# Optimization experiments

Hardware: AMD Instinct MI355X
Metric: run time of the kernel (lower is better)

Reference implementation:

```python
import jax, jax.numpy as jnp
import numpy as np
from jax import lax

NFILT = 80
NBINS = 257  # nfft//2 + 1


def build_filterbank(binpoints):
    """Vectorized version of the nested-loop triangular filterbank build.
    Matches torch semantics: bin ranges use int() (trunc==floor for positive
    values) of the sorted learnable binpoints; last filter row (j=nfilt-1)
    is never written and stays zero.
    """
    b = jnp.sort(binpoints)
    ib = jnp.floor(b).astype(jnp.int32)
    i = jnp.arange(NBINS)
    fi = i.astype(b.dtype)
    bj, bj1, bj2 = b[:NFILT, None], b[1:NFILT + 1, None], b[2:NFILT + 2, None]
    ibj, ibj1, ibj2 = ib[:NFILT, None], ib[1:NFILT + 1, None], ib[2:NFILT + 2, None]
    rise_m = (i >= ibj) & (i < ibj1)
    fall_m = (i >= ibj1) & (i < ibj2)
    d1 = (bj1 - bj) ** 2
    d2 = (bj2 - bj1) ** 2
    rise = (fi - bj) / jnp.where(d1 > 0, d1, 1.0)
    fall = (bj2 - fi) / jnp.where(d2 > 0, d2, 1.0)
    fb = jnp.where(rise_m, rise, jnp.where(fall_m, fall, 0.0))
    row_ok = (jnp.arange(NFILT) < NFILT - 1)[:, None]  # loop runs j in [0, nfilt-1)
    return fb * row_ok  # [80, 257]


def dconv1d(h, w, b, dilation, pad):
    # h: [B, C, T], w: [O, I, K]
    y = lax.conv_general_dilated(h, w, window_strides=(1,), padding=[(pad, pad)],
                                 rhs_dilation=(dilation,),
                                 dimension_numbers=('NCH', 'OIH', 'NCH'))
    return y + b[None, :, None]


def setup_inputs() -> dict:
    key = jax.random.key(0)
    ks = jax.random.split(key, 20)
    B, T = 64, 3000
    f32 = jnp.float32
    x = jax.random.normal(ks[0], (B, T, NBINS), dtype=f32)
    # distinct sorted binpoints in [1, 257) as in torch init (randint then sort)
    binpoints = jnp.sort(jax.random.choice(ks[1], jnp.arange(1, NBINS), (NFILT + 2,), replace=False).astype(f32))
    def lin(k, o, i):
        return jax.random.normal(k, (o, i), dtype=f32) * (1.0 / np.sqrt(i))
    def conv_w(k, o, i, ksz):
        return jax.random.normal(k, (o, i, ksz), dtype=f32) * (1.0 / np.sqrt(i * ksz))
    return {
        'x': x,
        'binpoints': binpoints,
        'w_lin1': lin(ks[2], 64, 80), 'b_lin1': jnp.zeros((64,), f32),
        'w_conv1': conv_w(ks[3], 128, 64, 3), 'b_conv1': jnp.zeros((128,), f32),
        'w_conv2': conv_w(ks[4], 128, 128, 3), 'b_conv2': jnp.zeros((128,), f32),
        'w_conv3': conv_w(ks[5], 128, 128, 3), 'b_conv3': jnp.zeros((128,), f32),
        'w_asp1': lin(ks[6], 64, 128), 'b_asp1': jnp.zeros((64,), f32),
        'w_asp2': lin(ks[7], 128, 64), 'b_asp2': jnp.zeros((128,), f32),
        'gamma': jnp.ones((256,), f32), 'beta': jnp.zeros((256,), f32),
        'w_lin2': lin(ks[8], 512, 256), 'b_lin2': jnp.zeros((512,), f32),
    }


def reference(x, binpoints, w_lin1, b_lin1, w_conv1, b_conv1, w_conv2, b_conv2,
              w_conv3, b_conv3, w_asp1, b_asp1, w_asp2, b_asp2, gamma, beta,
              w_lin2, b_lin2):
    fb = build_filterbank(binpoints)                       # [80, 257]
    filt = jnp.einsum('btf,nf->btn', x, fb)                # [B, T, 80]
    filt = filt.at[:, :, 0].set(x[:, :, 0])               # restore first column
    # remove_zero_rows: with dense random input no row sums to exactly 0 -> identity
    h = jax.nn.relu(jnp.einsum('btn,on->bto', filt, w_lin1) + b_lin1)  # [B, T, 64]
    h = jnp.transpose(h, (0, 2, 1))                        # [B, 64, T]
    i1 = dconv1d(h, w_conv1, b_conv1, 2, 2)
    i2 = dconv1d(i1, w_conv2, b_conv2, 3, 3) + i1
    i3 = dconv1d(i1 + i2, w_conv3, b_conv3, 4, 4) + i1 + i2  # [B, 128, T]
    # Attentive stats pooling (1x1 convs == per-timestep linear)
    a = jnp.tanh(jnp.einsum('bct,oc->bot', i3, w_asp1) + b_asp1[None, :, None])
    a = jnp.einsum('bct,oc->bot', a, w_asp2) + b_asp2[None, :, None]
    alpha = jax.nn.softmax(a, axis=2)                      # [B, 128, T]
    mean = jnp.sum(alpha * i3, axis=2)
    resid = jnp.sum(alpha * i3 ** 2, axis=2) - mean ** 2
    std = jnp.sqrt(jnp.clip(resid, 1e-9))
    out = jnp.concatenate([mean, std], axis=1)             # [B, 256]
    # GroupNorm(1, 256) on [B, C]
    mu = jnp.mean(out, axis=1, keepdims=True)
    var = jnp.var(out, axis=1, keepdims=True)
    out = (out - mu) / jnp.sqrt(var + 1e-5) * gamma + beta
    return out @ w_lin2.T + b_lin2                         # [B, 512]
```

## Files before the change

kernel.cpp:

```cpp
#include <hip/hip_runtime.h>
#include <math.h>


constexpr int B_  = 64;
constexpr int T_  = 3000;
constexpr int NB_ = 257;
constexpr int R_  = B_ * T_;
constexpr int NCH = 24;

constexpr size_t OFF_BS    = 0;
constexpr size_t OFF_WEFF  = 128;
constexpr size_t OFF_WTAIL = OFF_WEFF + 20480;
constexpr size_t OFF_W1    = OFF_WTAIL + 128;
constexpr size_t OFF_W2    = OFF_W1  + 3*64*128;
constexpr size_t OFF_W3    = OFF_W2  + 3*128*128;
constexpr size_t OFF_WA1   = OFF_W3  + 3*128*128;
constexpr size_t OFF_WA2   = OFF_WA1 + 8192;
constexpr size_t SZ_P      = (size_t)B_*NCH*128;
constexpr size_t OFF_PM    = OFF_WA2 + 8192;
constexpr size_t OFF_PS    = OFF_PM  + SZ_P;
constexpr size_t OFF_PCM   = OFF_PS  + SZ_P;
constexpr size_t OFF_PCQ   = OFF_PCM + SZ_P;
constexpr size_t OFF_HS    = OFF_PCQ + SZ_P;
constexpr size_t OFF_AS    = OFF_HS  + (size_t)R_*32;
constexpr size_t OFF_SLACK = OFF_AS  + (size_t)R_*64;
constexpr size_t OFF_WL2T  = OFF_SLACK + 4096;

typedef __attribute__((ext_vector_type(8))) short  bf16x8;
typedef __attribute__((ext_vector_type(4))) float  f32x4;
typedef __attribute__((ext_vector_type(4), aligned(4))) float float4a;
typedef unsigned short ushort_t;

typedef __attribute__((address_space(3))) unsigned int        as3_u32;
typedef const __attribute__((address_space(1))) unsigned int  as1_u32c;
__device__ __forceinline__ void gload16(const void* g, void* l) {
    __builtin_amdgcn_global_load_lds((as1_u32c*)g, (as3_u32*)l, 16, 0, 0);
}

__device__ inline ushort_t f2bf(float f) {
    unsigned u = __float_as_uint(f);
    unsigned r = u + 0x7FFFu + ((u >> 16) & 1u);
    return (ushort_t)(r >> 16);
}
__device__ inline float bf2f(ushort_t h) {
    return __uint_as_float(((unsigned)h) << 16);
}
__device__ inline void split2(float v, ushort_t &h, ushort_t &l) {
    h = f2bf(v);
    l = f2bf(v - bf2f(h));
}

__device__ inline float fast_tanh(float x) {
    float cx = fminf(fmaxf(x, -15.0f), 15.0f);
    float e  = __expf(2.0f * cx);
    return __fdividef(e - 1.0f, e + 1.0f);
}

__device__ inline void pack_hi4(float x, float y, float z, float w, uint2 &ph) {
    unsigned hx, hy;
    asm("v_cvt_pk_bf16_f32 %0, %1, %2" : "=v"(hx) : "v"(x), "v"(y));
    asm("v_cvt_pk_bf16_f32 %0, %1, %2" : "=v"(hy) : "v"(z), "v"(w));
    ph.x = hx; ph.y = hy;
}

__global__ void sort_kernel(const float* __restrict__ bp, float* __restrict__ bs) {
    if (threadIdx.x == 0) {
        float tmp[82];
        for (int i = 0; i < 82; ++i) tmp[i] = bp[i];
        for (int i = 1; i < 82; ++i) {
            float key = tmp[i];
            int j = i - 1;
            while (j >= 0 && tmp[j] > key) { tmp[j+1] = tmp[j]; --j; }
            tmp[j+1] = key;
        }
        for (int i = 0; i < 82; ++i) bs[i] = tmp[i];
    }
}

__global__ void prep_kernel(const float* __restrict__ bs, const float* __restrict__ wl1,
                            const float* __restrict__ wc1, const float* __restrict__ wc2,
                            const float* __restrict__ wc3, const float* __restrict__ wa1,
                            const float* __restrict__ wa2, const float* __restrict__ wl2,
                            ushort_t* __restrict__ weh, ushort_t* __restrict__ wel,
                            float* __restrict__ wtail,
                            ushort_t* __restrict__ w1h, ushort_t* __restrict__ w1l,
                            ushort_t* __restrict__ w2h, ushort_t* __restrict__ w2l,
                            ushort_t* __restrict__ w3h, ushort_t* __restrict__ w3l,
                            ushort_t* __restrict__ wa1h, ushort_t* __restrict__ wa1l,
                            ushort_t* __restrict__ wa2h, ushort_t* __restrict__ wa2l,
                            float* __restrict__ wl2t) {
    int gid = blockIdx.x * 256 + threadIdx.x;
    if (gid < 64*320) {
        int o = gid / 320, f = gid % 320;
        if (f > 256) return;
        float acc = 0.0f;
        if (f == 0) acc = wl1[o*80];
        else {
            for (int n = 1; n < 79; ++n) {
                float bn = bs[n], bn1 = bs[n+1], bn2 = bs[n+2];
                int ibn  = (int)floorf(bn);
                int ibn1 = (int)floorf(bn1);
                int ibn2 = (int)floorf(bn2);
                float fbv = 0.0f;
                if (f >= ibn && f < ibn1) {
                    float d = (bn1-bn)*(bn1-bn);
                    fbv = ((float)f - bn) / (d > 0.0f ? d : 1.0f);
                } else if (f >= ibn1 && f < ibn2) {
                    float d = (bn2-bn1)*(bn2-bn1);
                    fbv = (bn2 - (float)f) / (d > 0.0f ? d : 1.0f);
                }
                acc += wl1[o*80 + n] * fbv;
            }
        }
        if (f == 256) { wtail[o] = acc; return; }
        int kc = f >> 5, lane = ((f & 31) >> 3)*16 + (o & 15), e = f & 7;
        size_t dst = (((size_t)kc*4 + (o >> 4))*64 + lane)*8 + e;
        split2(acc, weh[dst], wel[dst]);
        return;
    }
    gid -= 64*320;
    if (gid < 3*128*64) {
        int k = gid / (128*64), rem = gid % (128*64);
        int c = rem >> 6, ci = rem & 63;
        float v = wc1[(c*64 + ci)*3 + k];
        int lane = ((ci & 31) >> 3)*16 + (c & 15), e = ci & 7;
        size_t dst = ((((size_t)k*2 + (ci >> 5))*8 + (c >> 4))*64 + lane)*8 + e;
        split2(v, w1h[dst], w1l[dst]);
        return;
    }
    gid -= 3*128*64;
    if (gid < 3*128*128) {
        int k = gid / (128*128), rem = gid % (128*128);
        int c = rem >> 7, ci = rem & 127;
        float v = wc2[(c*128 + ci)*3 + k];
        int lane = ((ci & 31) >> 3)*16 + (c & 15), e = ci & 7;
        size_t dst = ((((size_t)k*4 + (ci >> 5))*8 + (c >> 4))*64 + lane)*8 + e;
        split2(v, w2h[dst], w2l[dst]);
        return;
    }
    gid -= 3*128*128;
    if (gid < 3*128*128) {
        int k = gid / (128*128), rem = gid % (128*128);
        int c = rem >> 7, ci = rem & 127;
        float v = wc3[(c*128 + ci)*3 + k];
        int lane = ((ci & 31) >> 3)*16 + (c & 15), e = ci & 7;
        size_t dst = ((((size_t)k*4 + (ci >> 5))*8 + (c >> 4))*64 + lane)*8 + e;
        split2(v, w3h[dst], w3l[dst]);
        return;
    }
    gid -= 3*128*128;
    if (gid < 64*128) {
        int c = gid >> 7, ci = gid & 127;
        float v = wa1[gid];
        int lane = ((ci & 31) >> 3)*16 + (c & 15), e = ci & 7;
        size_t dst = (((size_t)(ci >> 5)*4 + (c >> 4))*64 + lane)*8 + e;
        split2(v, wa1h[dst], wa1l[dst]);
        return;
    }
    gid -= 64*128;
    if (gid < 128*64) {
        int n = gid >> 6, ci = gid & 63;
        float v = wa2[gid];
        int lane = ((ci & 31) >> 3)*16 + (n & 15), e = ci & 7;
        size_t dst = (((size_t)(ci >> 5)*8 + (n >> 4))*64 + lane)*8 + e;
        split2(v, wa2h[dst], wa2l[dst]);
        return;
    }
    gid -= 128*64;
    if (gid < 256*512) {
        int j = gid >> 9, o = gid & 511;
        wl2t[gid] = wl2[(size_t)o*256 + j];
        return;
    }
}

__launch_bounds__(256)
__global__ void lin1_mfma(const float* __restrict__ X,
                          const ushort_t* __restrict__ Wh, const ushort_t* __restrict__ Wl,
                          const float* __restrict__ wtail,
                          const float* __restrict__ bias,
                          ushort_t* __restrict__ Hs) {
    __shared__ __align__(16) ushort_t ash[128*64];
    __shared__ float xs[128];
    __shared__ float wts[64];
    const int tid  = threadIdx.x;
    const int lane = tid & 63;
    const int wid  = tid >> 6;
    const int wy   = wid >> 1, wx = wid & 1;
    const int l16  = lane & 15, l4 = lane >> 4;
    const int r0   = blockIdx.x * 128;

    if (tid < 128)       xs[tid] = X[(size_t)(r0 + tid)*NB_ + 256];
    else if (tid < 192)  wts[tid - 128] = wtail[tid - 128];

#define LIN1_LOAD(dst, k0)                                            \
    _Pragma("unroll")                                                 \
    for (int i = 0; i < 8; ++i) {                                     \
        int q = tid + i*256; int r = q >> 4, cc = (q & 15) << 2;      \
        dst[i] = *(const float4a*)(X + (size_t)(r0 + r)*NB_ + (k0) + cc); \
    }
#define LIN1_CW(src)                                                  \
    _Pragma("unroll")                                                 \
    for (int i = 0; i < 8; ++i) {                                     \
        int q = tid + i*256; int r = q >> 4, cc = (q & 15) << 2;      \
        uint2 ph;                                                     \
        pack_hi4(src[i].x, src[i].y, src[i].z, src[i].w, ph);         \
        unsigned byte = ((unsigned)(r*64 + cc))*2u ^ ((unsigned)((r & 7) << 4)); \
        *(uint2*)((char*)ash + byte) = ph;                            \
    }

    float4a bufA[8], bufB[8];
    LIN1_LOAD(bufA, 0);

    f32x4 acc[4][2];
    const f32x4 z = {0.f,0.f,0.f,0.f};
#pragma unroll
    for (int m = 0; m < 4; ++m) { acc[m][0] = z; acc[m][1] = z; }

#pragma unroll
    for (int ck = 0; ck < 4; ++ck) {
        const float4a* cur = (ck & 1) ? bufB : bufA;
        float4a*       nxt = (ck & 1) ? bufA : bufB;
        if (ck < 3) LIN1_LOAD(nxt, (ck + 1)*64);
        LIN1_CW(cur);
        __syncthreads();
#pragma unroll
        for (int kk = 0; kk < 64; kk += 32) {
            bf16x8 bh[2], bl[2];
#pragma unroll
            for (int n = 0; n < 2; ++n) {
                size_t off = (((size_t)(ck*2 + (kk >> 5))*4 + wx*2 + n)*64 + lane)*8;
                bh[n] = *(const bf16x8*)(Wh + off);
                bl[n] = *(const bf16x8*)(Wl + off);
            }
            bf16x8 fh[4];
#pragma unroll
            for (int m = 0; m < 4; ++m) {
                int r = wy*64 + m*16 + l16;
                unsigned byte = ((unsigned)(r*64 + kk + l4*8))*2u ^ ((unsigned)((r & 7) << 4));
                fh[m] = *(const bf16x8*)((const char*)ash + byte);
            }
#pragma unroll
            for (int m = 0; m < 4; ++m)
#pragma unroll
                for (int n = 0; n < 2; ++n) {
                    acc[m][n] = __builtin_amdgcn_mfma_f32_16x16x32_bf16(fh[m], bh[n], acc[m][n], 0, 0, 0);
                    acc[m][n] = __builtin_amdgcn_mfma_f32_16x16x32_bf16(fh[m], bl[n], acc[m][n], 0, 0, 0);
                }
        }
        __syncthreads();
    }
#undef LIN1_LOAD
#undef LIN1_CW

#pragma unroll
    for (int m = 0; m < 4; ++m)
#pragma unroll
        for (int n = 0; n < 2; ++n) {
            int c = wx*32 + n*16 + l16;
            float bv = bias[c];
            float wc = wts[c];
            int rbl = wy*64 + m*16 + l4*4;
#pragma unroll
            for (int rg = 0; rg < 4; ++rg) {
                int rl = rbl + rg;
                float v = fmaxf(acc[m][n][rg] + bv + xs[rl]*wc, 0.0f);
                Hs[(size_t)(r0 + rl)*64 + c] = f2bf(v);
            }
        }
}

__launch_bounds__(256, 4)
__global__ void dconv1_mfma(const ushort_t* __restrict__ Xs,
                            const ushort_t* __restrict__ Wh, const ushort_t* __restrict__ Wl,
                            const float* __restrict__ bias,
                            ushort_t* __restrict__ Ys) {
    constexpr int CIN = 64, DIL = 2;
    constexpr int TT  = 64;
    constexpr int HS  = TT + 2*DIL;
    constexpr int NCK = HS*8;
    constexpr int NCKP = ((NCK + 255)/256)*256;
    __shared__ __align__(16) ushort_t hs_[NCKP*8];

    const int tid  = threadIdx.x;
    const int lane = tid & 63;
    const int wid  = tid >> 6;
    const int l16  = lane & 15;
    const int l4   = lane >> 4;
    const int t0   = blockIdx.x * TT;
    const int b    = blockIdx.y;

    const long long rowbase = ((long long)b*T_ + (t0 - DIL)) * CIN;
    for (int c0 = wid*64; c0 < NCKP; c0 += 256) {
        int ck = c0 + lane;
        int r  = ck >> 3;
        int sc = ck ^ (r & 7);
        gload16(Xs + rowbase + (long long)sc*8, (char*)hs_ + (size_t)c0*16);
    }
    __syncthreads();
    if (t0 < DIL || t0 + TT + DIL > T_) {
        for (int idx = tid; idx < HS*CIN/4; idx += 256) {
            int e = idx << 2;
            int r = e / CIN, ci = e % CIN;
            int t = t0 - DIL + r;
            if (t < 0 || t >= T_) {
                unsigned byte = ((unsigned)(r*CIN + ci))*2u ^ ((unsigned)((r & 7) << 4));
                *(uint2*)((char*)hs_ + byte) = make_uint2(0u, 0u);
            }
        }
        __syncthreads();
    }

    f32x4 acc[4][2];
    const f32x4 z = {0.f, 0.f, 0.f, 0.f};
#pragma unroll
    for (int m = 0; m < 4; ++m)
#pragma unroll
        for (int n = 0; n < 2; ++n) acc[m][n] = z;

#pragma unroll
    for (int k = 0; k < 3; ++k) {
#pragma unroll
        for (int cb = 0; cb < 2; ++cb) {
            bf16x8 bh[2], bl[2];
#pragma unroll
            for (int n = 0; n < 2; ++n) {
                size_t off = ((((size_t)k*2 + cb)*8 + wid*2 + n)*64 + lane)*8;
                bh[n] = *(const bf16x8*)(Wh + off);
                bl[n] = *(const bf16x8*)(Wl + off);
            }
            bf16x8 ah[4];
#pragma unroll
            for (int m = 0; m < 4; ++m) {
                int r = m*16 + l16 + k*DIL;
                unsigned byte = ((unsigned)(r*CIN + cb*32 + l4*8))*2u
                              ^ ((unsigned)((r & 7) << 4));
                ah[m] = *(const bf16x8*)((const char*)hs_ + byte);
            }
#pragma unroll
            for (int m = 0; m < 4; ++m)
#pragma unroll
                for (int n = 0; n < 2; ++n) {
                    acc[m][n] = __builtin_amdgcn_mfma_f32_16x16x32_bf16(ah[m], bh[n], acc[m][n], 0, 0, 0);
                    acc[m][n] = __builtin_amdgcn_mfma_f32_16x16x32_bf16(ah[m], bl[n], acc[m][n], 0, 0, 0);
                }
        }
    }

#pragma unroll
    for (int m = 0; m < 4; ++m) {
        int tl_base = m*16 + l4*4;
#pragma unroll
        for (int n = 0; n < 2; ++n) {
            int c = wid*32 + n*16 + l16;
            float bv = bias[c];
#pragma unroll
            for (int rg = 0; rg < 4; ++rg) {
                int tl = tl_base + rg;
                int t  = t0 + tl;
                if (t < T_) {
                    float v = acc[m][n][rg] + bv;
                    Ys[((size_t)b*T_ + t)*128 + c] = f2bf(v);
                }
            }
        }
    }
}

__launch_bounds__(512)
__global__ void dconv23_asp(const ushort_t* __restrict__ Xs,
                            const ushort_t* __restrict__ W2h, const ushort_t* __restrict__ W2l,
                            const ushort_t* __restrict__ W3h, const ushort_t* __restrict__ W3l,
                            const float* __restrict__ bc2, const float* __restrict__ bc3,
                            const ushort_t* __restrict__ Wa1h, const ushort_t* __restrict__ Wa1l,
                            const ushort_t* __restrict__ Wa2h, const ushort_t* __restrict__ Wa2l,
                            const float* __restrict__ ba1, const float* __restrict__ ba2,
                            float* __restrict__ pm, float* __restrict__ ps,
                            float* __restrict__ pcm, float* __restrict__ pcq) {
    __shared__ __align__(16) char smem[73728];
    ushort_t* i1s = (ushort_t*)smem;
    ushort_t* ss_ = (ushort_t*)(smem + 36864);
    ushort_t* vs_ = (ushort_t*)smem;

    const int tid  = threadIdx.x;
    const int lane = tid & 63;
    const int wid  = tid >> 6;
    const int l16  = lane & 15, l4 = lane >> 4;
    const int ch   = blockIdx.x;
    const int b    = blockIdx.y;
    const int t0   = ch * 128;

    const long long rowbase = ((long long)b*T_ + (t0 - 8)) * 128;
    for (int c0 = wid*64; c0 < 2304; c0 += 512) {
        int ck = c0 + lane;
        int r  = ck >> 4;
        int sc = ck ^ (r & 15);
        gload16(Xs + rowbase + (long long)sc*8, (char*)i1s + (size_t)c0*16);
    }
    __syncthreads();
    if (t0 < 8 || t0 + 136 > T_) {
        for (int idx = tid; idx < 144*128/4; idx += 512) {
            int e = idx << 2;
            int r = e >> 7, ci = e & 127;
            int t = t0 - 8 + r;
            if (t < 0 || t >= T_) {
                unsigned byte = ((unsigned)(r*128 + ci))*2u ^ ((unsigned)((r & 15) << 4));
                *(uint2*)((char*)i1s + byte) = make_uint2(0u, 0u);
            }
        }
        __syncthreads();
    }

    {
        f32x4 acc[9];
        const f32x4 z = {0.f,0.f,0.f,0.f};
#pragma unroll
        for (int m = 0; m < 9; ++m) acc[m] = z;
#pragma unroll
        for (int k = 0; k < 3; ++k) {
#pragma unroll
            for (int cb = 0; cb < 4; ++cb) {
                size_t off = ((((size_t)k*4 + cb)*8 + wid)*64 + lane)*8;
                bf16x8 bh = *(const bf16x8*)(W2h + off);
                bf16x8 bl = *(const bf16x8*)(W2l + off);
#pragma unroll
                for (int m = 0; m < 9; ++m) {
                    int r = m*16 + l16 + k*3 - 3;
                    r = min(max(r, 0), 143);
                    unsigned byte = ((unsigned)(r*128 + cb*32 + l4*8))*2u
                                  ^ ((unsigned)((r & 15) << 4));
                    bf16x8 ah = *(const bf16x8*)((const char*)i1s + byte);
                    acc[m] = __builtin_amdgcn_mfma_f32_16x16x32_bf16(ah, bh, acc[m], 0, 0, 0);
                    acc[m] = __builtin_amdgcn_mfma_f32_16x16x32_bf16(ah, bl, acc[m], 0, 0, 0);
                }
            }
        }
        const int c = wid*16 + l16;
        const float bv = bc2[c];
#pragma unroll
        for (int m = 0; m < 9; ++m) {
#pragma unroll
            for (int rg = 0; rg < 4; ++rg) {
                int rl = m*16 + l4*4 + rg;
                int t  = t0 - 8 + rl;
                float v = 0.0f;
                unsigned byte = ((unsigned)(rl*128 + c))*2u ^ ((unsigned)((rl & 15) << 4));
                if (t >= 0 && t < T_) {
                    float cen = bf2f(*(const ushort_t*)((const char*)i1s + byte));
                    v = acc[m][rg] + bv + 2.0f*cen;
                }
                *(ushort_t*)((char*)ss_ + byte) = f2bf(v);
            }
        }
    }
    __syncthreads();

    float i3r[8][4];
    {
        f32x4 acc[8];
        const f32x4 z = {0.f,0.f,0.f,0.f};
#pragma unroll
        for (int m = 0; m < 8; ++m) acc[m] = z;
#pragma unroll
        for (int k = 0; k < 3; ++k) {
#pragma unroll
            for (int cb = 0; cb < 4; ++cb) {
                size_t off = ((((size_t)k*4 + cb)*8 + wid)*64 + lane)*8;
                bf16x8 bh = *(const bf16x8*)(W3h + off);
                bf16x8 bl = *(const bf16x8*)(W3l + off);
#pragma unroll
                for (int m = 0; m < 8; ++m) {
                    int r = 8 + m*16 + l16 + k*4 - 4;
                    unsigned byte = ((unsigned)(r*128 + cb*32 + l4*8))*2u
                                  ^ ((unsigned)((r & 15) << 4));
                    bf16x8 ah = *(const bf16x8*)((const char*)ss_ + byte);
                    acc[m] = __builtin_amdgcn_mfma_f32_16x16x32_bf16(ah, bh, acc[m], 0, 0, 0);
                    acc[m] = __builtin_amdgcn_mfma_f32_16x16x32_bf16(ah, bl, acc[m], 0, 0, 0);
                }
            }
        }
        const int c = wid*16 + l16;
        const float bv = bc3[c];
#pragma unroll
        for (int m = 0; m < 8; ++m)
#pragma unroll
            for (int rg = 0; rg < 4; ++rg) {
                int rl = 8 + m*16 + l4*4 + rg;
                unsigned byte = ((unsigned)(rl*128 + c))*2u ^ ((unsigned)((rl & 15) << 4));
                float cen = bf2f(*(const ushort_t*)((const char*)ss_ + byte));
                i3r[m][rg] = acc[m][rg] + bv + cen;
            }
    }
    __syncthreads();
    {
        const int c = wid*16 + l16;
#pragma unroll
        for (int m = 0; m < 8; ++m)
#pragma unroll
            for (int rg = 0; rg < 4; ++rg) {
                int rl = 8 + m*16 + l4*4 + rg;
                unsigned byte = ((unsigned)(rl*128 + c))*2u ^ ((unsigned)((rl & 15) << 4));
                *(ushort_t*)((char*)ss_ + byte) = f2bf(i3r[m][rg]);
            }
    }
    __syncthreads();

    {
        const int wy = wid >> 2;
        const int wx = wid & 3;
        f32x4 acc1[4];
        const f32x4 z = {0.f,0.f,0.f,0.f};
#pragma unroll
        for (int m = 0; m < 4; ++m) acc1[m] = z;
#pragma unroll
        for (int kc = 0; kc < 4; ++kc) {
            size_t off = (((size_t)kc*4 + wx)*64 + lane)*8;
            bf16x8 bh = *(const bf16x8*)(Wa1h + off);
            bf16x8 bl = *(const bf16x8*)(Wa1l + off);
#pragma unroll
            for (int m = 0; m < 4; ++m) {
                int rl = 8 + wy*64 + m*16 + l16;
                unsigned byte = ((unsigned)(rl*128 + kc*32 + l4*8))*2u
                              ^ ((unsigned)((rl & 15) << 4));
                bf16x8 ah = *(const bf16x8*)((const char*)ss_ + byte);
                acc1[m] = __builtin_amdgcn_mfma_f32_16x16x32_bf16(ah, bh, acc1[m], 0, 0, 0);
                acc1[m] = __builtin_amdgcn_mfma_f32_16x16x32_bf16(ah, bl, acc1[m], 0, 0, 0);
            }
        }
        const int c = wx*16 + l16;
        const float bv = ba1[c];
#pragma unroll
        for (int m = 0; m < 4; ++m)
#pragma unroll
            for (int rg = 0; rg < 4; ++rg) {
                float v = fast_tanh(acc1[m][rg] + bv);
                int r = wy*64 + m*16 + l4*4 + rg;
                unsigned byte = ((unsigned)(r*64 + c))*2u ^ ((unsigned)((r & 7) << 4));
                *(ushort_t*)((char*)vs_ + byte) = f2bf(v);
            }
    }
    __syncthreads();

    {
        f32x4 acc2[8];
        const f32x4 z = {0.f,0.f,0.f,0.f};
#pragma unroll
        for (int j = 0; j < 8; ++j) acc2[j] = z;
#pragma unroll
        for (int kc = 0; kc < 2; ++kc) {
            size_t off = (((size_t)kc*8 + wid)*64 + lane)*8;
            bf16x8 awh = *(const bf16x8*)(Wa2h + off);
            bf16x8 awl = *(const bf16x8*)(Wa2l + off);
#pragma unroll
            for (int j = 0; j < 8; ++j) {
                int t = j*16 + l16;
                unsigned byte = ((unsigned)(t*64 + kc*32 + l4*8))*2u
                              ^ ((unsigned)((t & 7) << 4));
                bf16x8 bv_ = *(const bf16x8*)((const char*)vs_ + byte);
                acc2[j] = __builtin_amdgcn_mfma_f32_16x16x32_bf16(awh, bv_, acc2[j], 0, 0, 0);
                acc2[j] = __builtin_amdgcn_mfma_f32_16x16x32_bf16(awl, bv_, acc2[j], 0, 0, 0);
            }
        }
        const float4 bvv = *(const float4*)&ba2[wid*16 + l4*4];
        const float bva[4] = {bvv.x, bvv.y, bvv.z, bvv.w};
#pragma unroll
        for (int rg = 0; rg < 4; ++rg) {
            const int n = wid*16 + l4*4 + rg;
            float mx = -INFINITY;
#pragma unroll
            for (int j = 0; j < 8; ++j) {
                int tg = t0 + j*16 + l16;
                if (tg < T_) mx = fmaxf(mx, acc2[j][rg] + bva[rg]);
            }
            mx = fmaxf(mx, __shfl_xor(mx, 1));
            mx = fmaxf(mx, __shfl_xor(mx, 2));
            mx = fmaxf(mx, __shfl_xor(mx, 4));
            mx = fmaxf(mx, __shfl_xor(mx, 8));
            float se = 0.0f, am = 0.0f, aq = 0.0f;
#pragma unroll
            for (int j = 0; j < 8; ++j) {
                int tl = j*16 + l16;
                int tg = t0 + tl;
                if (tg < T_) {
                    float p = __expf(acc2[j][rg] + bva[rg] - mx);
                    int rl = tl + 8;
                    unsigned byte = ((unsigned)(rl*128 + n))*2u ^ ((unsigned)((rl & 15) << 4));
                    float x = bf2f(*(const ushort_t*)((const char*)ss_ + byte));
                    se += p; am += p*x; aq += p*x*x;
                }
            }
#pragma unroll
            for (int d = 1; d <= 8; d <<= 1) {
                se += __shfl_xor(se, d);
                am += __shfl_xor(am, d);
                aq += __shfl_xor(aq, d);
            }
            if (l16 == 0) {
                size_t o = ((size_t)b*NCH + ch)*128 + n;
                pm[o]  = mx;
                ps[o]  = se;
                pcm[o] = am;
                pcq[o] = aq;
            }
        }
    }
}

__launch_bounds__(256)
__global__ void final_kernel(const float* __restrict__ pcm, const float* __restrict__ pcq,
                             const float* __restrict__ pm, const float* __restrict__ ps,
                             const float* __restrict__ gamma, const float* __restrict__ beta,
                             const float* __restrict__ w2t, const float* __restrict__ b2,
                             float* __restrict__ out) {
    __shared__ float row[256];
    __shared__ float nrm[256];
    __shared__ float red[8];
    const int tid = threadIdx.x, b = blockIdx.x;
    if (tid < 128) {
        float M = -INFINITY;
        for (int ch = 0; ch < NCH; ++ch)
            M = fmaxf(M, pm[((size_t)b*NCH + ch)*128 + tid]);
        float S = 0.0f, sm = 0.0f, sq = 0.0f;
        for (int ch = 0; ch < NCH; ++ch) {
            size_t o = ((size_t)b*NCH + ch)*128 + tid;
            float m = pm[o];
            if (m > -INFINITY) {
                float e = expf(m - M);
                S  += ps[o]*e;
                sm += pcm[o]*e;
                sq += pcq[o]*e;
            }
        }
        float mean = sm / S;
        float q    = sq / S;
        float resid = q - mean*mean;
        float stdv  = sqrtf(fmaxf(resid, 1e-9f));
        row[tid]       = mean;
        row[128 + tid] = stdv;
    }
    __syncthreads();
    float v  = row[tid];
    float s1 = v, s2 = v*v;
    for (int off = 32; off >= 1; off >>= 1) {
        s1 += __shfl_down(s1, off, 64);
        s2 += __shfl_down(s2, off, 64);
    }
    if ((tid & 63) == 0) { red[tid >> 6] = s1; red[4 + (tid >> 6)] = s2; }
    __syncthreads();
    float S1 = red[0] + red[1] + red[2] + red[3];
    float S2 = red[4] + red[5] + red[6] + red[7];
    float mu  = S1 / 256.0f;
    float var = S2 / 256.0f - mu*mu;
    float inv = 1.0f / sqrtf(var + 1e-5f);
    nrm[tid] = (v - mu)*inv*gamma[tid] + beta[tid];
    __syncthreads();
    float acc0 = b2[tid], acc1 = b2[tid + 256];
#pragma unroll 4
    for (int j = 0; j < 256; ++j) {
        float nv = nrm[j];
        const float* wr = w2t + (size_t)j*512;
        acc0 += wr[tid]       * nv;
        acc1 += wr[tid + 256] * nv;
    }
    out[(size_t)b*512 + tid]       = acc0;
    out[(size_t)b*512 + tid + 256] = acc1;
}

extern "C" void kernel_launch(void* const* d_in, const int* in_sizes, int n_in,
                              void* d_out, int out_size, void* d_ws, size_t ws_size,
                              hipStream_t stream) {
    const float* x      = (const float*)d_in[0];
    const float* bp     = (const float*)d_in[1];
    const float* w_lin1 = (const float*)d_in[2];
    const float* b_lin1 = (const float*)d_in[3];
    const float* wc1    = (const float*)d_in[4];
    const float* bc1    = (const float*)d_in[5];
    const float* wc2    = (const float*)d_in[6];
    const float* bc2    = (const float*)d_in[7];
    const float* wc3    = (const float*)d_in[8];
    const float* bc3    = (const float*)d_in[9];
    const float* wa1    = (const float*)d_in[10];
    const float* ba1    = (const float*)d_in[11];
    const float* wa2    = (const float*)d_in[12];
    const float* ba2    = (const float*)d_in[13];
    const float* gamma  = (const float*)d_in[14];
    const float* beta   = (const float*)d_in[15];
    const float* wl2    = (const float*)d_in[16];
    const float* bl2    = (const float*)d_in[17];

    float* ws   = (float*)d_ws;
    float* bs   = ws + OFF_BS;
    ushort_t* weh  = (ushort_t*)(ws + OFF_WEFF);
    ushort_t* wel  = weh + 64*320;
    float* wtail   = ws + OFF_WTAIL;
    ushort_t* w1h  = (ushort_t*)(ws + OFF_W1);
    ushort_t* w1l  = w1h + 3*128*64;
    ushort_t* w2h  = (ushort_t*)(ws + OFF_W2);
    ushort_t* w2l  = w2h + 3*128*128;
    ushort_t* w3h  = (ushort_t*)(ws + OFF_W3);
    ushort_t* w3l  = w3h + 3*128*128;
    ushort_t* wa1h = (ushort_t*)(ws + OFF_WA1);
    ushort_t* wa1l = wa1h + 64*128;
    ushort_t* wa2h = (ushort_t*)(ws + OFF_WA2);
    ushort_t* wa2l = wa2h + 128*64;
    float* pm   = ws + OFF_PM;
    float* ps   = ws + OFF_PS;
    float* pcm  = ws + OFF_PCM;
    float* pcq  = ws + OFF_PCQ;
    ushort_t* Hs = (ushort_t*)(ws + OFF_HS);
    ushort_t* As = (ushort_t*)(ws + OFF_AS);
    float* wl2t  = ws + OFF_WL2T;

    sort_kernel<<<dim3(1), dim3(64), 0, stream>>>(bp, bs);
    prep_kernel<<<dim3(1136), dim3(256), 0, stream>>>(bs, w_lin1, wc1, wc2, wc3, wa1, wa2,
                                                      wl2, weh, wel, wtail, w1h, w1l,
                                                      w2h, w2l, w3h, w3l, wa1h, wa1l,
                                                      wa2h, wa2l, wl2t);
    lin1_mfma<<<dim3(R_/128), dim3(256), 0, stream>>>(x, weh, wel, wtail, b_lin1, Hs);
    dconv1_mfma<<<dim3(47, B_), dim3(256), 0, stream>>>(Hs, w1h, w1l, bc1, As);
    dconv23_asp<<<dim3(NCH, B_), dim3(512), 0, stream>>>(As, w2h, w2l, w3h, w3l,
                                                         bc2, bc3, wa1h, wa1l,
                                                         wa2h, wa2l, ba1, ba2,
                                                         pm, ps, pcm, pcq);
    final_kernel<<<dim3(B_), dim3(256), 0, stream>>>(pcm, pcq, pm, ps, gamma, beta,
                                                     wl2t, bl2, (float*)d_out);
}
```

Measured before the change: 289.6 us.

## Fuse first dilated conv into the conv2/conv3/attention-pooling kernel

Removes the standalone dconv1 kernel and computes conv1 inside the fused conv2/conv3/ASP kernel. Each 128-step tile loads its slice of the lin1 output with a 10-step halo into shared memory and writes the conv1 result with an 8-step halo straight into the shared buffer that conv2 reads. This avoids writing the 128-channel bf16 intermediate to global memory and reading it back, and drops one launch. In exchange the halo rows of conv1 are computed redundantly in every tile, and the shared-memory regions are reassigned so the buffers can alias.

```diff
diff --git a/kernel.cpp b/kernel.cpp
--- a/kernel.cpp
+++ b/kernel.cpp
@@ -23,8 +23,7 @@
 constexpr size_t OFF_PCQ   = OFF_PCM + SZ_P;
 constexpr size_t OFF_HS    = OFF_PCQ + SZ_P;
 constexpr size_t OFF_AS    = OFF_HS  + (size_t)R_*32;
-constexpr size_t OFF_SLACK = OFF_AS  + (size_t)R_*64;
-constexpr size_t OFF_WL2T  = OFF_SLACK + 4096;
+constexpr size_t OFF_WL2T  = OFF_AS  + (size_t)R_*64 + 4096;
 
 typedef __attribute__((ext_vector_type(8))) short  bf16x8;
 typedef __attribute__((ext_vector_type(4))) float  f32x4;
@@ -270,117 +269,23 @@
         }
 }
 
-__launch_bounds__(256, 4)
-__global__ void dconv1_mfma(const ushort_t* __restrict__ Xs,
-                            const ushort_t* __restrict__ Wh, const ushort_t* __restrict__ Wl,
-                            const float* __restrict__ bias,
-                            ushort_t* __restrict__ Ys) {
-    constexpr int CIN = 64, DIL = 2;
-    constexpr int TT  = 64;
-    constexpr int HS  = TT + 2*DIL;
-    constexpr int NCK = HS*8;
-    constexpr int NCKP = ((NCK + 255)/256)*256;
-    __shared__ __align__(16) ushort_t hs_[NCKP*8];
-
-    const int tid  = threadIdx.x;
-    const int lane = tid & 63;
-    const int wid  = tid >> 6;
-    const int l16  = lane & 15;
-    const int l4   = lane >> 4;
-    const int t0   = blockIdx.x * TT;
-    const int b    = blockIdx.y;
-
-    const long long rowbase = ((long long)b*T_ + (t0 - DIL)) * CIN;
-    for (int c0 = wid*64; c0 < NCKP; c0 += 256) {
-        int ck = c0 + lane;
-        int r  = ck >> 3;
-        int sc = ck ^ (r & 7);
-        gload16(Xs + rowbase + (long long)sc*8, (char*)hs_ + (size_t)c0*16);
-    }
-    __syncthreads();
-    if (t0 < DIL || t0 + TT + DIL > T_) {
-        for (int idx = tid; idx < HS*CIN/4; idx += 256) {
-            int e = idx << 2;
-            int r = e / CIN, ci = e % CIN;
-            int t = t0 - DIL + r;
-            if (t < 0 || t >= T_) {
-                unsigned byte = ((unsigned)(r*CIN + ci))*2u ^ ((unsigned)((r & 7) << 4));
-                *(uint2*)((char*)hs_ + byte) = make_uint2(0u, 0u);
-            }
-        }
-        __syncthreads();
-    }
-
-    f32x4 acc[4][2];
-    const f32x4 z = {0.f, 0.f, 0.f, 0.f};
-#pragma unroll
-    for (int m = 0; m < 4; ++m)
-#pragma unroll
-        for (int n = 0; n < 2; ++n) acc[m][n] = z;
-
-#pragma unroll
-    for (int k = 0; k < 3; ++k) {
-#pragma unroll
-        for (int cb = 0; cb < 2; ++cb) {
-            bf16x8 bh[2], bl[2];
-#pragma unroll
-            for (int n = 0; n < 2; ++n) {
-                size_t off = ((((size_t)k*2 + cb)*8 + wid*2 + n)*64 + lane)*8;
-                bh[n] = *(const bf16x8*)(Wh + off);
-                bl[n] = *(const bf16x8*)(Wl + off);
-            }
-            bf16x8 ah[4];
-#pragma unroll
-            for (int m = 0; m < 4; ++m) {
-                int r = m*16 + l16 + k*DIL;
-                unsigned byte = ((unsigned)(r*CIN + cb*32 + l4*8))*2u
-                              ^ ((unsigned)((r & 7) << 4));
-                ah[m] = *(const bf16x8*)((const char*)hs_ + byte);
-            }
-#pragma unroll
-            for (int m = 0; m < 4; ++m)
-#pragma unroll
-                for (int n = 0; n < 2; ++n) {
-                    acc[m][n] = __builtin_amdgcn_mfma_f32_16x16x32_bf16(ah[m], bh[n], acc[m][n], 0, 0, 0);
-                    acc[m][n] = __builtin_amdgcn_mfma_f32_16x16x32_bf16(ah[m], bl[n], acc[m][n], 0, 0, 0);
-                }
-        }
-    }
-
-#pragma unroll
-    for (int m = 0; m < 4; ++m) {
-        int tl_base = m*16 + l4*4;
-#pragma unroll
-        for (int n = 0; n < 2; ++n) {
-            int c = wid*32 + n*16 + l16;
-            float bv = bias[c];
-#pragma unroll
-            for (int rg = 0; rg < 4; ++rg) {
-                int tl = tl_base + rg;
-                int t  = t0 + tl;
-                if (t < T_) {
-                    float v = acc[m][n][rg] + bv;
-                    Ys[((size_t)b*T_ + t)*128 + c] = f2bf(v);
-                }
-            }
-        }
-    }
-}
-
 __launch_bounds__(512)
-__global__ void dconv23_asp(const ushort_t* __restrict__ Xs,
-                            const ushort_t* __restrict__ W2h, const ushort_t* __restrict__ W2l,
-                            const ushort_t* __restrict__ W3h, const ushort_t* __restrict__ W3l,
-                            const float* __restrict__ bc2, const float* __restrict__ bc3,
-                            const ushort_t* __restrict__ Wa1h, const ushort_t* __restrict__ Wa1l,
-                            const ushort_t* __restrict__ Wa2h, const ushort_t* __restrict__ Wa2l,
-                            const float* __restrict__ ba1, const float* __restrict__ ba2,
-                            float* __restrict__ pm, float* __restrict__ ps,
-                            float* __restrict__ pcm, float* __restrict__ pcq) {
+__global__ void dconv123_asp(const ushort_t* __restrict__ Hs,
+                             const ushort_t* __restrict__ W1h, const ushort_t* __restrict__ W1l,
+                             const ushort_t* __restrict__ W2h, const ushort_t* __restrict__ W2l,
+                             const ushort_t* __restrict__ W3h, const ushort_t* __restrict__ W3l,
+                             const float* __restrict__ bc1, const float* __restrict__ bc2,
+                             const float* __restrict__ bc3,
+                             const ushort_t* __restrict__ Wa1h, const ushort_t* __restrict__ Wa1l,
+                             const ushort_t* __restrict__ Wa2h, const ushort_t* __restrict__ Wa2l,
+                             const float* __restrict__ ba1, const float* __restrict__ ba2,
+                             float* __restrict__ pm, float* __restrict__ ps,
+                             float* __restrict__ pcm, float* __restrict__ pcq) {
     __shared__ __align__(16) char smem[73728];
-    ushort_t* i1s = (ushort_t*)smem;
-    ushort_t* ss_ = (ushort_t*)(smem + 36864);
-    ushort_t* vs_ = (ushort_t*)smem;
+    ushort_t* hs_ = (ushort_t*)smem;
+    ushort_t* ss_ = (ushort_t*)smem;
+    ushort_t* i1s = (ushort_t*)(smem + 36864);
+    ushort_t* vs_ = (ushort_t*)(smem + 36864);
 
     const int tid  = threadIdx.x;
     const int lane = tid & 63;
@@ -390,26 +295,65 @@
     const int b    = blockIdx.y;
     const int t0   = ch * 128;
 
-    const long long rowbase = ((long long)b*T_ + (t0 - 8)) * 128;
-    for (int c0 = wid*64; c0 < 2304; c0 += 512) {
+    const long long rowbase_h = ((long long)b*T_ + (t0 - 10)) * 64;
+    for (int c0 = wid*64; c0 < 1280; c0 += 512) {
         int ck = c0 + lane;
-        int r  = ck >> 4;
-        int sc = ck ^ (r & 15);
-        gload16(Xs + rowbase + (long long)sc*8, (char*)i1s + (size_t)c0*16);
-    }
-    __syncthreads();
-    if (t0 < 8 || t0 + 136 > T_) {
-        for (int idx = tid; idx < 144*128/4; idx += 512) {
+        int r  = ck >> 3;
+        int sc = ck ^ (r & 7);
+        gload16(Hs + rowbase_h + (long long)sc*8, (char*)hs_ + (size_t)c0*16);
+    }
+    __syncthreads();
+    if (t0 < 10 || t0 + 138 > T_) {
+        for (int idx = tid; idx < 148*64/4; idx += 512) {
             int e = idx << 2;
-            int r = e >> 7, ci = e & 127;
-            int t = t0 - 8 + r;
+            int r = e >> 6, ci = e & 63;
+            int t = t0 - 10 + r;
             if (t < 0 || t >= T_) {
-                unsigned byte = ((unsigned)(r*128 + ci))*2u ^ ((unsigned)((r & 15) << 4));
-                *(uint2*)((char*)i1s + byte) = make_uint2(0u, 0u);
+                unsigned byte = ((unsigned)(r*64 + ci))*2u ^ ((unsigned)((r & 7) << 4));
+                *(uint2*)((char*)hs_ + byte) = make_uint2(0u, 0u);
             }
         }
         __syncthreads();
     }
+
+    {
+        f32x4 acc[9];
+        const f32x4 z = {0.f,0.f,0.f,0.f};
+#pragma unroll
+        for (int m = 0; m < 9; ++m) acc[m] = z;
+#pragma unroll
+        for (int k = 0; k < 3; ++k) {
+#pragma unroll
+            for (int cb = 0; cb < 2; ++cb) {
+                size_t off = ((((size_t)k*2 + cb)*8 + wid)*64 + lane)*8;
+                bf16x8 bh = *(const bf16x8*)(W1h + off);
+                bf16x8 bl = *(const bf16x8*)(W1l + off);
+#pragma unroll
+                for (int m = 0; m < 9; ++m) {
+                    int r = m*16 + l16 + 2*k;
+                    unsigned byte = ((unsigned)(r*64 + cb*32 + l4*8))*2u
+                                  ^ ((unsigned)((r & 7) << 4));
+                    bf16x8 ah = *(const bf16x8*)((const char*)hs_ + byte);
+                    acc[m] = __builtin_amdgcn_mfma_f32_16x16x32_bf16(ah, bh, acc[m], 0, 0, 0);
+                    acc[m] = __builtin_amdgcn_mfma_f32_16x16x32_bf16(ah, bl, acc[m], 0, 0, 0);
+                }
+            }
+        }
+        const int c = wid*16 + l16;
+        const float bv = bc1[c];
+#pragma unroll
+        for (int m = 0; m < 9; ++m) {
+#pragma unroll
+            for (int rg = 0; rg < 4; ++rg) {
+                int rl = m*16 + l4*4 + rg;
+                int t  = t0 - 8 + rl;
+                float v = (t >= 0 && t < T_) ? (acc[m][rg] + bv) : 0.0f;
+                unsigned byte = ((unsigned)(rl*128 + c))*2u ^ ((unsigned)((rl & 15) << 4));
+                *(ushort_t*)((char*)i1s + byte) = f2bf(v);
+            }
+        }
+    }
+    __syncthreads();
 
     {
         f32x4 acc[9];
@@ -708,7 +652,6 @@
     float* pcm  = ws + OFF_PCM;
     float* pcq  = ws + OFF_PCQ;
     ushort_t* Hs = (ushort_t*)(ws + OFF_HS);
-    ushort_t* As = (ushort_t*)(ws + OFF_AS);
     float* wl2t  = ws + OFF_WL2T;
 
     sort_kernel<<<dim3(1), dim3(64), 0, stream>>>(bp, bs);
@@ -717,11 +660,10 @@
                                                       w2h, w2l, w3h, w3l, wa1h, wa1l,
                                                       wa2h, wa2l, wl2t);
     lin1_mfma<<<dim3(R_/128), dim3(256), 0, stream>>>(x, weh, wel, wtail, b_lin1, Hs);
-    dconv1_mfma<<<dim3(47, B_), dim3(256), 0, stream>>>(Hs, w1h, w1l, bc1, As);
-    dconv23_asp<<<dim3(NCH, B_), dim3(512), 0, stream>>>(As, w2h, w2l, w3h, w3l,
-                                                         bc2, bc3, wa1h, wa1l,
-                                                         wa2h, wa2l, ba1, ba2,
-                                                         pm, ps, pcm, pcq);
+    dconv123_asp<<<dim3(NCH, B_), dim3(512), 0, stream>>>(Hs, w1h, w1l, w2h, w2l,
+                                                          w3h, w3l, bc1, bc2, bc3,
+                                                          wa1h, wa1l, wa2h, wa2l,
+                                                          ba1, ba2, pm, ps, pcm, pcq);
     final_kernel<<<dim3(B_), dim3(256), 0, stream>>>(pcm, pcq, pm, ps, gamma, beta,
                                                      wl2t, bl2, (float*)d_out);
 }
```

New measurement: 263.3 us (median of 2 runs). -9.1%, faster.
